# Performance work log

Measured on AMD Instinct MI355X. Metric: run time of the kernel, lower is better.

## Reference

```python
import jax, jax.numpy as jnp
import numpy as np

N_GAUSS = 1024
IMG = 192
TANFOV = 0.5  # tan(FoV/2), both axes
ZNEAR, ZFAR = 0.01, 100.0

C0 = 0.28209479177387814
C1 = 0.4886025119029199
C2 = (1.0925484305920792, -1.0925484305920792, 0.31539156525252005, -1.0925484305920792, 0.5462742152960396)
C3 = (-0.5900435899266435, 2.890611442640554, -0.4570457994644658, 0.3731763325901154, -0.4570457994644658, 1.445305721320277, -0.5900435899266435)


def _eval_sh3(sh, d):
    # sh: [N,16,3] coeffs, d: [N,3] unit dirs -> clamped rgb [N,3]
    x, y, z = d[:, 0:1], d[:, 1:2], d[:, 2:3]
    xx, yy, zz = x * x, y * y, z * z
    xy, yz, xz = x * y, y * z, x * z
    res = (C0 * sh[:, 0]
           - C1 * y * sh[:, 1] + C1 * z * sh[:, 2] - C1 * x * sh[:, 3]
           + C2[0] * xy * sh[:, 4] + C2[1] * yz * sh[:, 5]
           + C2[2] * (2.0 * zz - xx - yy) * sh[:, 6]
           + C2[3] * xz * sh[:, 7] + C2[4] * (xx - yy) * sh[:, 8]
           + C3[0] * y * (3.0 * xx - yy) * sh[:, 9]
           + C3[1] * xy * z * sh[:, 10]
           + C3[2] * y * (4.0 * zz - xx - yy) * sh[:, 11]
           + C3[3] * z * (2.0 * zz - 3.0 * xx - 3.0 * yy) * sh[:, 12]
           + C3[4] * x * (4.0 * zz - xx - yy) * sh[:, 13]
           + C3[5] * z * (xx - yy) * sh[:, 14]
           + C3[6] * x * (xx - yy - 3.0 * zz) * sh[:, 15])
    return jnp.maximum(res + 0.5, 0.0)


def _quat_to_rot(q):
    r, x, y, z = q[:, 0], q[:, 1], q[:, 2], q[:, 3]
    return jnp.stack([
        1 - 2 * (y * y + z * z), 2 * (x * y - r * z), 2 * (x * z + r * y),
        2 * (x * y + r * z), 1 - 2 * (x * x + z * z), 2 * (y * z - r * x),
        2 * (x * z - r * y), 2 * (y * z + r * x), 1 - 2 * (x * x + y * y),
    ], axis=-1).reshape(-1, 3, 3)


def setup_inputs() -> dict:
    key = jax.random.key(0)
    ks = jax.random.split(key, 6)
    xy = jax.random.uniform(ks[0], (N_GAUSS, 2), minval=-2.0, maxval=2.0)
    z = jax.random.uniform(ks[1], (N_GAUSS, 1), minval=2.0, maxval=10.0)
    means3D = jnp.concatenate([xy, z], axis=1)
    scales = jax.random.uniform(ks[2], (N_GAUSS, 3), minval=0.01, maxval=0.08)
    q = jax.random.normal(ks[3], (N_GAUSS, 4))
    rotations = q / jnp.linalg.norm(q, axis=1, keepdims=True)
    opacities = jax.random.uniform(ks[4], (N_GAUSS, 1), minval=0.1, maxval=0.99)
    shs = jax.random.normal(ks[5], (N_GAUSS, 16, 3)) * 0.3
    viewmatrix = jnp.eye(4, dtype=jnp.float32)
    proj = np.zeros((4, 4), np.float32)
    proj[0, 0] = 1.0 / TANFOV
    proj[1, 1] = 1.0 / TANFOV
    proj[2, 2] = ZFAR / (ZFAR - ZNEAR)
    proj[2, 3] = -ZFAR * ZNEAR / (ZFAR - ZNEAR)
    proj[3, 2] = 1.0
    return dict(means3D=means3D, scales=scales, rotations=rotations,
                opacities=opacities, shs=shs, viewmatrix=viewmatrix,
                projmatrix=jnp.asarray(proj), campos=jnp.zeros(3, jnp.float32),
                bg_color=jnp.zeros(3, jnp.float32),
                image_height=IMG, image_width=IMG)


def reference(means3D, scales, rotations, opacities, shs, viewmatrix,
              projmatrix, campos, bg_color, image_height, image_width):
    H, W = int(image_height), int(image_width)
    fx = W / (2.0 * TANFOV)
    fy = H / (2.0 * TANFOV)
    N = means3D.shape[0]

    # SH -> RGB (convert_SHs_python branch, active_sh_degree = 3)
    dir_pp = means3D - campos[None, :]
    dir_pp = dir_pp / jnp.linalg.norm(dir_pp, axis=1, keepdims=True)
    colors = _eval_sh3(shs, dir_pp)  # [N,3]

    # 3D covariance Sigma = (R S)(R S)^T  (scale_modifier = 1.0)
    R = _quat_to_rot(rotations)
    M = R * scales[:, None, :]
    cov3d = jnp.einsum('nij,nkj->nik', M, M)  # [N,3,3]

    # projection of means
    hom = jnp.concatenate([means3D, jnp.ones((N, 1), means3D.dtype)], axis=1)
    p_view = hom @ viewmatrix.T
    depth = p_view[:, 2]
    p_hom = hom @ projmatrix.T
    p_proj = p_hom[:, :3] / (p_hom[:, 3:4] + 1e-7)
    gx = ((p_proj[:, 0] + 1.0) * W - 1.0) * 0.5  # ndc2Pix
    gy = ((p_proj[:, 1] + 1.0) * H - 1.0) * 0.5
    means2D = jnp.stack([gx, gy], axis=1)

    in_front = depth > 0.2
    tz = jnp.where(in_front, depth, 1.0)
    lim = 1.3 * TANFOV
    tx = jnp.clip(p_view[:, 0] / tz, -lim, lim) * tz
    ty = jnp.clip(p_view[:, 1] / tz, -lim, lim) * tz

    # EWA splatting: J (top 2 rows) composed with view rotation
    zeros = jnp.zeros_like(tz)
    J = jnp.stack([
        jnp.stack([fx / tz, zeros, -fx * tx / (tz * tz)], axis=-1),
        jnp.stack([zeros, fy / tz, -fy * ty / (tz * tz)], axis=-1),
    ], axis=1)  # [N,2,3]
    T = jnp.einsum('nij,jk->nik', J, viewmatrix[:3, :3])
    cov2d = jnp.einsum('nij,njk,nlk->nil', T, cov3d, T)  # [N,2,2]
    a = cov2d[:, 0, 0] + 0.3  # low-pass filter on diagonal
    b = cov2d[:, 0, 1]
    c = cov2d[:, 1, 1] + 0.3

    det = a * c - b * b
    pos_det = det > 0
    inv_det = jnp.where(pos_det, 1.0 / jnp.where(pos_det, det, 1.0), 0.0)
    conA, conB, conC = c * inv_det, -b * inv_det, a * inv_det

    mid = 0.5 * (a + c)
    lam = mid + jnp.sqrt(jnp.maximum(mid * mid - det, 0.1))
    visible = in_front & pos_det
    radii = jnp.where(visible, jnp.ceil(3.0 * jnp.sqrt(lam)), 0.0)
    visibility_filter = radii > 0

    # per-pixel depth-sorted alpha compositing (dense stand-in for tiles)
    yy, xx = jnp.meshgrid(jnp.arange(H, dtype=means3D.dtype),
                          jnp.arange(W, dtype=means3D.dtype), indexing='ij')
    px = xx.reshape(-1)
    py = yy.reshape(-1)
    dx = gx[None, :] - px[:, None]  # [P,N]
    dy = gy[None, :] - py[:, None]
    power = (-0.5 * (conA[None, :] * dx * dx + conC[None, :] * dy * dy)
             - conB[None, :] * dx * dy)
    keep = ((jnp.abs(dx) <= radii[None, :]) & (jnp.abs(dy) <= radii[None, :])
            & visible[None, :] & (power <= 0.0))
    alpha = jnp.minimum(0.99, opacities[:, 0][None, :] * jnp.exp(jnp.minimum(power, 0.0)))
    alpha = jnp.where(keep & (alpha >= 1.0 / 255.0), alpha, 0.0)

    order = jnp.argsort(jnp.where(visible, depth, jnp.inf))
    a_s = alpha[:, order]
    Tcum = jnp.cumprod(1.0 - a_s, axis=1)
    T_before = jnp.concatenate(
        [jnp.ones((a_s.shape[0], 1), a_s.dtype), Tcum[:, :-1]], axis=1)
    wgt = a_s * T_before
    img = wgt @ colors[order] + Tcum[:, -1:] * bg_color[None, :]
    rendered = img.reshape(H, W, 3).transpose(2, 0, 1)  # CHW like torch
    return rendered, radii.astype(jnp.int32), visibility_filter, means2D
```

## Files before the change

kernel.cpp:

```cpp
#include <hip/hip_runtime.h>

#define NG      1024
#define W_IMG   192
#define H_IMG   192
#define HW      (W_IMG * H_IMG)
#define PSTR    12
#define NSEG    8
#define SEGLEN  (NG / NSEG)
#define TILES_X (W_IMG / 8)
#define TILES_Y (H_IMG / 8)
#define NTILES  (TILES_X * TILES_Y)


__global__ __launch_bounds__(64) void preprocess_kernel(
    const float* __restrict__ means3D, const float* __restrict__ scales,
    const float* __restrict__ rotations, const float* __restrict__ opacities,
    const float* __restrict__ shs, const float* __restrict__ viewm,
    const float* __restrict__ projm, const float* __restrict__ campos,
    float* __restrict__ params, float* __restrict__ keys,
    float* __restrict__ outp)
{
    const int i = blockIdx.x * 64 + threadIdx.x;
    if (i >= NG) return;

    const float mx = means3D[i * 3 + 0];
    const float my = means3D[i * 3 + 1];
    const float mz = means3D[i * 3 + 2];

    float dxc = mx - campos[0], dyc = my - campos[1], dzc = mz - campos[2];
    float nrm = sqrtf(dxc * dxc + dyc * dyc + dzc * dzc);
    float x = dxc / nrm, y = dyc / nrm, z = dzc / nrm;
    float xx = x * x, yy = y * y, zz = z * z;
    float xy = x * y, yz = y * z, xz = x * z;

    float basis[16];
    basis[0]  = 0.28209479177387814f;
    basis[1]  = -0.4886025119029199f * y;
    basis[2]  =  0.4886025119029199f * z;
    basis[3]  = -0.4886025119029199f * x;
    basis[4]  =  1.0925484305920792f * xy;
    basis[5]  = -1.0925484305920792f * yz;
    basis[6]  =  0.31539156525252005f * (2.f * zz - xx - yy);
    basis[7]  = -1.0925484305920792f * xz;
    basis[8]  =  0.5462742152960396f * (xx - yy);
    basis[9]  = -0.5900435899266435f * y * (3.f * xx - yy);
    basis[10] =  2.890611442640554f  * xy * z;
    basis[11] = -0.4570457994644658f * y * (4.f * zz - xx - yy);
    basis[12] =  0.3731763325901154f * z * (2.f * zz - 3.f * xx - 3.f * yy);
    basis[13] = -0.4570457994644658f * x * (4.f * zz - xx - yy);
    basis[14] =  1.445305721320277f  * z * (xx - yy);
    basis[15] = -0.5900435899266435f * x * (xx - yy - 3.f * zz);

    float cr = 0.f, cg = 0.f, cb = 0.f;
#pragma unroll
    for (int k = 0; k < 16; ++k) {
        float b = basis[k];
        cr += b * shs[(i * 16 + k) * 3 + 0];
        cg += b * shs[(i * 16 + k) * 3 + 1];
        cb += b * shs[(i * 16 + k) * 3 + 2];
    }
    cr = fmaxf(cr + 0.5f, 0.f);
    cg = fmaxf(cg + 0.5f, 0.f);
    cb = fmaxf(cb + 0.5f, 0.f);

    float qr = rotations[i * 4 + 0], qx = rotations[i * 4 + 1];
    float qy = rotations[i * 4 + 2], qz = rotations[i * 4 + 3];
    float sx = scales[i * 3 + 0], sy = scales[i * 3 + 1], sz = scales[i * 3 + 2];
    float R00 = 1.f - 2.f * (qy * qy + qz * qz), R01 = 2.f * (qx * qy - qr * qz), R02 = 2.f * (qx * qz + qr * qy);
    float R10 = 2.f * (qx * qy + qr * qz), R11 = 1.f - 2.f * (qx * qx + qz * qz), R12 = 2.f * (qy * qz - qr * qx);
    float R20 = 2.f * (qx * qz - qr * qy), R21 = 2.f * (qy * qz + qr * qx), R22 = 1.f - 2.f * (qx * qx + qy * qy);
    float M00 = R00 * sx, M01 = R01 * sy, M02 = R02 * sz;
    float M10 = R10 * sx, M11 = R11 * sy, M12 = R12 * sz;
    float M20 = R20 * sx, M21 = R21 * sy, M22 = R22 * sz;
    float S00 = M00 * M00 + M01 * M01 + M02 * M02;
    float S01 = M00 * M10 + M01 * M11 + M02 * M12;
    float S02 = M00 * M20 + M01 * M21 + M02 * M22;
    float S11 = M10 * M10 + M11 * M11 + M12 * M12;
    float S12 = M10 * M20 + M11 * M21 + M12 * M22;
    float S22 = M20 * M20 + M21 * M21 + M22 * M22;

    float pv0 = viewm[0] * mx + viewm[1] * my + viewm[2]  * mz + viewm[3];
    float pv1 = viewm[4] * mx + viewm[5] * my + viewm[6]  * mz + viewm[7];
    float pv2 = viewm[8] * mx + viewm[9] * my + viewm[10] * mz + viewm[11];
    float ph0 = projm[0]  * mx + projm[1]  * my + projm[2]  * mz + projm[3];
    float ph1 = projm[4]  * mx + projm[5]  * my + projm[6]  * mz + projm[7];
    float ph3 = projm[12] * mx + projm[13] * my + projm[14] * mz + projm[15];
    float pp0 = ph0 / (ph3 + 1e-7f);
    float pp1 = ph1 / (ph3 + 1e-7f);
    float gx = ((pp0 + 1.f) * (float)W_IMG - 1.f) * 0.5f;
    float gy = ((pp1 + 1.f) * (float)H_IMG - 1.f) * 0.5f;

    float depth = pv2;
    bool in_front = depth > 0.2f;
    float tz = in_front ? depth : 1.f;
    const float lim = 1.3f * 0.5f;
    float txv = fminf(fmaxf(pv0 / tz, -lim), lim) * tz;
    float tyv = fminf(fmaxf(pv1 / tz, -lim), lim) * tz;
    const float fx = (float)W_IMG / (2.f * 0.5f);
    const float fy = (float)H_IMG / (2.f * 0.5f);
    float J00 = fx / tz, J02 = -fx * txv / (tz * tz);
    float J11 = fy / tz, J12 = -fy * tyv / (tz * tz);

    float T00 = J00 * viewm[0] + J02 * viewm[8];
    float T01 = J00 * viewm[1] + J02 * viewm[9];
    float T02 = J00 * viewm[2] + J02 * viewm[10];
    float T10 = J11 * viewm[4] + J12 * viewm[8];
    float T11 = J11 * viewm[5] + J12 * viewm[9];
    float T12 = J11 * viewm[6] + J12 * viewm[10];

    float u0 = T00 * S00 + T01 * S01 + T02 * S02;
    float u1 = T00 * S01 + T01 * S11 + T02 * S12;
    float u2 = T00 * S02 + T01 * S12 + T02 * S22;
    float v0 = T10 * S00 + T11 * S01 + T12 * S02;
    float v1 = T10 * S01 + T11 * S11 + T12 * S12;
    float v2 = T10 * S02 + T11 * S12 + T12 * S22;
    float c00 = u0 * T00 + u1 * T01 + u2 * T02;
    float c01 = u0 * T10 + u1 * T11 + u2 * T12;
    float c11 = v0 * T10 + v1 * T11 + v2 * T12;

    float a = c00 + 0.3f;
    float b = c01;
    float c = c11 + 0.3f;
    float det = a * c - b * b;
    bool pos_det = det > 0.f;
    float inv_det = pos_det ? 1.f / det : 0.f;
    float conA = c * inv_det, conB = -b * inv_det, conC = a * inv_det;
    float mid = 0.5f * (a + c);
    float lam = mid + sqrtf(fmaxf(mid * mid - det, 0.1f));
    bool visible = in_front && pos_det;
    float radii = visible ? ceilf(3.f * sqrtf(lam)) : 0.f;

    float opa = opacities[i];

    outp[3 * HW + i] = radii;
    outp[3 * HW + NG + i] = (radii > 0.f) ? 1.f : 0.f;
    outp[3 * HW + 2 * NG + i * 2 + 0] = gx;
    outp[3 * HW + 2 * NG + i * 2 + 1] = gy;

    float* p = params + i * PSTR;
    p[0] = gx;   p[1] = gy;   p[2]  = radii; p[3]  = visible ? opa : 0.f;
    p[4] = conA; p[5] = conB; p[6]  = conC;  p[7]  = 0.f;
    p[8] = cr;   p[9] = cg;   p[10] = cb;    p[11] = 0.f;

    keys[i] = visible ? depth : 1e30f;
}

__global__ __launch_bounds__(64) void sort_kernel(
    const float* __restrict__ keys, const float* __restrict__ params,
    float* __restrict__ sorted)
{
    const int i = blockIdx.x;
    const int lane = threadIdx.x;
    const float ki = keys[i];
    int cnt = 0;
#pragma unroll
    for (int k = 0; k < NG / 64; ++k) {
        int j = lane + k * 64;
        float kj = keys[j];
        cnt += (kj < ki || (kj == ki && j < i)) ? 1 : 0;
    }
    for (int off = 32; off > 0; off >>= 1) cnt += __shfl_down(cnt, off);
    int rank = __shfl(cnt, 0);
    if (lane < PSTR) sorted[rank * PSTR + lane] = params[i * PSTR + lane];
}

__global__ __launch_bounds__(512) void raster_kernel(
    const float* __restrict__ sorted, const float* __restrict__ bg,
    float* __restrict__ outp)
{
    __shared__ float4 sp[NG * 3];
    __shared__ float4 segacc[NSEG * 64];

    const int t = threadIdx.x;
    {
        const float4* src = (const float4*)sorted;
        for (int k = t; k < NG * 3; k += 512) sp[k] = src[k];
    }
    __syncthreads();

    const int wave = t >> 6;
    const int lane = t & 63;
    const int tileX = blockIdx.x % TILES_X;
    const int tileY = blockIdx.x / TILES_X;
    const int lx = lane & 7, ly = lane >> 3;
    const int pxi = tileX * 8 + lx;
    const int pyi = tileY * 8 + ly;
    const float px = (float)pxi, py = (float)pyi;
    const float tx0 = (float)(tileX * 8);
    const float ty0 = (float)(tileY * 8);

    const int base = wave * SEGLEN;

    unsigned long long m[2];
#pragma unroll
    for (int h = 0; h < 2; ++h) {
        float4 g0 = sp[(base + h * 64 + lane) * 3];
        bool hit = (g0.x >= tx0 - g0.z) && (g0.x <= tx0 + 7.f + g0.z) &&
                   (g0.y >= ty0 - g0.z) && (g0.y <= ty0 + 7.f + g0.z);
        m[h] = __ballot(hit);
    }

    float T = 1.f, accR = 0.f, accG = 0.f, accB = 0.f;
#pragma unroll
    for (int h = 0; h < 2; ++h) {
        unsigned long long mask = m[h];
        while (mask) {
            const int j = __ffsll(mask) - 1;
            mask &= mask - 1;
            const int gi = base + h * 64 + j;
            float4 g0 = sp[gi * 3 + 0];
            float4 g1 = sp[gi * 3 + 1];
            float4 g2 = sp[gi * 3 + 2];
            float dx = g0.x - px, dy = g0.y - py;
            bool cover = (fabsf(dx) <= g0.z) && (fabsf(dy) <= g0.z);
            float power = -0.5f * (g1.x * dx * dx + g1.z * dy * dy) - g1.y * dx * dy;
            float alpha = fminf(0.99f, g0.w * __expf(fminf(power, 0.f)));
            bool keep = cover && (power <= 0.f) && (alpha >= (1.f / 255.f));
            alpha = keep ? alpha : 0.f;
            float w = alpha * T;
            accR += w * g2.x;
            accG += w * g2.y;
            accB += w * g2.z;
            T *= (1.f - alpha);
        }
    }

    segacc[wave * 64 + lane] = make_float4(accR, accG, accB, T);
    __syncthreads();

    if (t < 64) {
        float Tc = 1.f, r = 0.f, g = 0.f, b = 0.f;
#pragma unroll
        for (int s = 0; s < NSEG; ++s) {
            float4 cc = segacc[s * 64 + t];
            r += Tc * cc.x;
            g += Tc * cc.y;
            b += Tc * cc.z;
            Tc *= cc.w;
        }
        const int pix = pyi * W_IMG + pxi;
        outp[pix]          = r + Tc * bg[0];
        outp[HW + pix]     = g + Tc * bg[1];
        outp[2 * HW + pix] = b + Tc * bg[2];
    }
}

extern "C" void kernel_launch(void* const* d_in, const int* in_sizes, int n_in,
                              void* d_out, int out_size, void* d_ws, size_t ws_size,
                              hipStream_t stream)
{
    const float* means3D   = (const float*)d_in[0];
    const float* scales    = (const float*)d_in[1];
    const float* rotations = (const float*)d_in[2];
    const float* opacities = (const float*)d_in[3];
    const float* shs       = (const float*)d_in[4];
    const float* viewm     = (const float*)d_in[5];
    const float* projm     = (const float*)d_in[6];
    const float* campos    = (const float*)d_in[7];
    const float* bg        = (const float*)d_in[8];

    float* outp   = (float*)d_out;
    float* params = (float*)d_ws;
    float* sorted = params + NG * PSTR;
    float* keys   = sorted + NG * PSTR;

    preprocess_kernel<<<NG / 64, 64, 0, stream>>>(
        means3D, scales, rotations, opacities, shs, viewm, projm, campos,
        params, keys, outp);

    sort_kernel<<<NG, 64, 0, stream>>>(keys, params, sorted);

    raster_kernel<<<NTILES, 512, 0, stream>>>(sorted, bg, outp);
}
```

Before: 85.18 us.

## Fuse global depth sort into raster kernel as per-tile culled rank sort

```diff
diff --git a/kernel.cpp b/kernel.cpp
--- a/kernel.cpp
+++ b/kernel.cpp
@@ -6,21 +6,19 @@
 #define HW      (W_IMG * H_IMG)
 #define PSTR    12
 #define NSEG    8
-#define SEGLEN  (NG / NSEG)
 #define TILES_X (W_IMG / 8)
 #define TILES_Y (H_IMG / 8)
 #define NTILES  (TILES_X * TILES_Y)
 
 
-__global__ __launch_bounds__(64) void preprocess_kernel(
+__global__ __launch_bounds__(256) void preprocess_kernel(
     const float* __restrict__ means3D, const float* __restrict__ scales,
     const float* __restrict__ rotations, const float* __restrict__ opacities,
     const float* __restrict__ shs, const float* __restrict__ viewm,
     const float* __restrict__ projm, const float* __restrict__ campos,
-    float* __restrict__ params, float* __restrict__ keys,
-    float* __restrict__ outp)
+    float* __restrict__ params, float* __restrict__ outp)
 {
-    const int i = blockIdx.x * 64 + threadIdx.x;
+    const int i = blockIdx.x * 256 + threadIdx.x;
     if (i >= NG) return;
 
     const float mx = means3D[i * 3 + 0];
@@ -139,41 +137,25 @@
 
     float* p = params + i * PSTR;
     p[0] = gx;   p[1] = gy;   p[2]  = radii; p[3]  = visible ? opa : 0.f;
-    p[4] = conA; p[5] = conB; p[6]  = conC;  p[7]  = 0.f;
+    p[4] = conA; p[5] = conB; p[6]  = conC;  p[7]  = visible ? depth : 1e30f;
     p[8] = cr;   p[9] = cg;   p[10] = cb;    p[11] = 0.f;
-
-    keys[i] = visible ? depth : 1e30f;
 }
 
-__global__ __launch_bounds__(64) void sort_kernel(
-    const float* __restrict__ keys, const float* __restrict__ params,
-    float* __restrict__ sorted)
-{
-    const int i = blockIdx.x;
-    const int lane = threadIdx.x;
-    const float ki = keys[i];
-    int cnt = 0;
-#pragma unroll
-    for (int k = 0; k < NG / 64; ++k) {
-        int j = lane + k * 64;
-        float kj = keys[j];
-        cnt += (kj < ki || (kj == ki && j < i)) ? 1 : 0;
-    }
-    for (int off = 32; off > 0; off >>= 1) cnt += __shfl_down(cnt, off);
-    int rank = __shfl(cnt, 0);
-    if (lane < PSTR) sorted[rank * PSTR + lane] = params[i * PSTR + lane];
-}
-
 __global__ __launch_bounds__(512) void raster_kernel(
-    const float* __restrict__ sorted, const float* __restrict__ bg,
+    const float* __restrict__ params, const float* __restrict__ bg,
     float* __restrict__ outp)
 {
     __shared__ float4 sp[NG * 3];
+    __shared__ float  sdep[NG];
+    __shared__ int    sidx[NG];
+    __shared__ int    ssorted[NG];
     __shared__ float4 segacc[NSEG * 64];
+    __shared__ int    s_cnt;
 
     const int t = threadIdx.x;
+    if (t == 0) s_cnt = 0;
     {
-        const float4* src = (const float4*)sorted;
+        const float4* src = (const float4*)params;
         for (int k = t; k < NG * 3; k += 512) sp[k] = src[k];
     }
     __syncthreads();
@@ -182,47 +164,69 @@
     const int lane = t & 63;
     const int tileX = blockIdx.x % TILES_X;
     const int tileY = blockIdx.x / TILES_X;
+    const float tx0 = (float)(tileX * 8);
+    const float ty0 = (float)(tileY * 8);
+
+#pragma unroll
+    for (int h = 0; h < 2; ++h) {
+        const int gi = wave * 128 + h * 64 + lane;
+        float4 g0 = sp[gi * 3];
+        bool hit = (g0.w > 0.f) &&
+                   (g0.x >= tx0 - g0.z) && (g0.x <= tx0 + 7.f + g0.z) &&
+                   (g0.y >= ty0 - g0.z) && (g0.y <= ty0 + 7.f + g0.z);
+        unsigned long long mask = __ballot(hit);
+        int base = 0;
+        if (lane == 0 && mask) base = atomicAdd(&s_cnt, __popcll(mask));
+        base = __shfl(base, 0);
+        if (hit) {
+            int pos = base + __popcll(mask & ((1ULL << lane) - 1ULL));
+            sidx[pos] = gi;
+            sdep[pos] = sp[gi * 3 + 1].w;
+        }
+    }
+    __syncthreads();
+
+    const int M = s_cnt;
+
+    for (int s = t; s < M; s += 512) {
+        const float ds = sdep[s];
+        const int   is = sidx[s];
+        int rank = 0;
+        for (int j = 0; j < M; ++j) {
+            float dj = sdep[j];
+            int   ij = sidx[j];
+            rank += (dj < ds || (dj == ds && ij < is)) ? 1 : 0;
+        }
+        ssorted[rank] = is;
+    }
+    __syncthreads();
+
     const int lx = lane & 7, ly = lane >> 3;
     const int pxi = tileX * 8 + lx;
     const int pyi = tileY * 8 + ly;
     const float px = (float)pxi, py = (float)pyi;
-    const float tx0 = (float)(tileX * 8);
-    const float ty0 = (float)(tileY * 8);
-
-    const int base = wave * SEGLEN;
-
-    unsigned long long m[2];
-#pragma unroll
-    for (int h = 0; h < 2; ++h) {
-        float4 g0 = sp[(base + h * 64 + lane) * 3];
-        bool hit = (g0.x >= tx0 - g0.z) && (g0.x <= tx0 + 7.f + g0.z) &&
-                   (g0.y >= ty0 - g0.z) && (g0.y <= ty0 + 7.f + g0.z);
-        m[h] = __ballot(hit);
-    }
+
+    const int chunk = (M + NSEG - 1) / NSEG;
+    const int kbeg = wave * chunk;
+    const int kend = min(M, kbeg + chunk);
 
     float T = 1.f, accR = 0.f, accG = 0.f, accB = 0.f;
-#pragma unroll
-    for (int h = 0; h < 2; ++h) {
-        unsigned long long mask = m[h];
-        while (mask) {
-            const int j = __ffsll(mask) - 1;
-            mask &= mask - 1;
-            const int gi = base + h * 64 + j;
-            float4 g0 = sp[gi * 3 + 0];
-            float4 g1 = sp[gi * 3 + 1];
-            float4 g2 = sp[gi * 3 + 2];
-            float dx = g0.x - px, dy = g0.y - py;
-            bool cover = (fabsf(dx) <= g0.z) && (fabsf(dy) <= g0.z);
-            float power = -0.5f * (g1.x * dx * dx + g1.z * dy * dy) - g1.y * dx * dy;
-            float alpha = fminf(0.99f, g0.w * __expf(fminf(power, 0.f)));
-            bool keep = cover && (power <= 0.f) && (alpha >= (1.f / 255.f));
-            alpha = keep ? alpha : 0.f;
-            float w = alpha * T;
-            accR += w * g2.x;
-            accG += w * g2.y;
-            accB += w * g2.z;
-            T *= (1.f - alpha);
-        }
+    for (int k = kbeg; k < kend; ++k) {
+        const int gi = ssorted[k];
+        float4 g0 = sp[gi * 3 + 0];
+        float4 g1 = sp[gi * 3 + 1];
+        float4 g2 = sp[gi * 3 + 2];
+        float dx = g0.x - px, dy = g0.y - py;
+        bool cover = (fabsf(dx) <= g0.z) && (fabsf(dy) <= g0.z);
+        float power = -0.5f * (g1.x * dx * dx + g1.z * dy * dy) - g1.y * dx * dy;
+        float alpha = fminf(0.99f, g0.w * __expf(fminf(power, 0.f)));
+        bool keep = cover && (power <= 0.f) && (alpha >= (1.f / 255.f));
+        alpha = keep ? alpha : 0.f;
+        float w = alpha * T;
+        accR += w * g2.x;
+        accG += w * g2.y;
+        accB += w * g2.z;
+        T *= (1.f - alpha);
     }
 
     segacc[wave * 64 + lane] = make_float4(accR, accG, accB, T);
@@ -261,14 +265,10 @@
 
     float* outp   = (float*)d_out;
     float* params = (float*)d_ws;
-    float* sorted = params + NG * PSTR;
-    float* keys   = sorted + NG * PSTR;
-
-    preprocess_kernel<<<NG / 64, 64, 0, stream>>>(
+
+    preprocess_kernel<<<NG / 256, 256, 0, stream>>>(
         means3D, scales, rotations, opacities, shs, viewm, projm, campos,
-        params, keys, outp);
-
-    sort_kernel<<<NG, 64, 0, stream>>>(keys, params, sorted);
-
-    raster_kernel<<<NTILES, 512, 0, stream>>>(sorted, bg, outp);
+        params, outp);
+
+    raster_kernel<<<NTILES, 512, 0, stream>>>(params, bg, outp);
 }
```

New measurement: 83.66 us. Within noise of the previous version (-1.8%).
